# Kernel tuning notes

Measured on AMD Instinct MI355X. Metric: run time of the kernel, lower is better.

The kernel has to match this reference:

```python
import jax, jax.numpy as jnp
import numpy as np

B, T, C, H = 4, 2048, 1024, 16
D = C // H  # head_size = 64


def _layernorm(x, g, b, eps=1e-5):
    mu = jnp.mean(x, axis=-1, keepdims=True)
    var = jnp.var(x, axis=-1, keepdims=True)
    return (x - mu) * jax.lax.rsqrt(var + eps) * g + b


def setup_inputs() -> dict:
    key = jax.random.key(0)
    ks = jax.random.split(key, 12)
    s = 0.02
    return {
        "x": jax.random.normal(ks[0], (B, T, C), dtype=jnp.float32),
        "Wq": jax.random.normal(ks[1], (C, C), dtype=jnp.float32) * s,
        "Wk": jax.random.normal(ks[2], (C, C), dtype=jnp.float32) * s,
        "Wv": jax.random.normal(ks[3], (C, C), dtype=jnp.float32) * s,
        "Wo": jax.random.normal(ks[4], (C, C), dtype=jnp.float32) * s,
        "bo": jnp.zeros((C,), dtype=jnp.float32),
        "ln1_g": jnp.ones((C,), dtype=jnp.float32),
        "ln1_b": jnp.zeros((C,), dtype=jnp.float32),
        "ln2_g": jnp.ones((C,), dtype=jnp.float32),
        "ln2_b": jnp.zeros((C,), dtype=jnp.float32),
        "W1": jax.random.normal(ks[5], (C, 4 * C), dtype=jnp.float32) * s,
        "b1": jnp.zeros((4 * C,), dtype=jnp.float32),
        "W2": jax.random.normal(ks[6], (4 * C, C), dtype=jnp.float32) * s,
        "b2": jnp.zeros((C,), dtype=jnp.float32),
    }


def reference(x, Wq, Wk, Wv, Wo, bo, ln1_g, ln1_b, ln2_g, ln2_b, W1, b1, W2, b2):
    # --- self-attention branch (pre-LN) ---
    h = _layernorm(x, ln1_g, ln1_b)
    q = (h @ Wq).reshape(B, T, H, D)
    k = (h @ Wk).reshape(B, T, H, D)
    v = (h @ Wv).reshape(B, T, H, D)
    scores = jnp.einsum("bqhd,bkhd->bhqk", q, k) * (D ** -0.5)
    causal = jnp.tril(jnp.ones((T, T), dtype=bool))
    scores = jnp.where(causal, scores, -jnp.inf)
    attn = jax.nn.softmax(scores, axis=-1)  # dropout=0 in eval
    out = jnp.einsum("bhqk,bkhd->bqhd", attn, v).reshape(B, T, C)
    x = x + (out @ Wo + bo)
    # --- feed-forward branch (pre-LN) ---
    h2 = _layernorm(x, ln2_g, ln2_b)
    ff = jax.nn.relu(h2 @ W1 + b1) @ W2 + b2
    return x + ff
```

## Files before the change

### kernel.cpp

```cpp
#include <hip/hip_runtime.h>
#include <hip/hip_bf16.h>
#include <math.h>

#define Bsz 4
#define Tsz 2048
#define Csz 1024
#define Hsz 16
#define Dsz 64
#define Msz (Bsz * Tsz)

typedef __attribute__((ext_vector_type(8))) __bf16 bf16x8;
typedef __attribute__((ext_vector_type(2))) __bf16 bf16x2;
typedef __attribute__((ext_vector_type(4))) float f32x4;

#define GLOBAL_AS __attribute__((address_space(1)))
#define LDS_AS    __attribute__((address_space(3)))

#if __has_builtin(__builtin_amdgcn_exp2f)
#define EXP2F(x) __builtin_amdgcn_exp2f(x)
#define HAVE_NATIVE_EXP2 1
#else
#define HAVE_NATIVE_EXP2 0
#endif


__device__ __forceinline__ float block_sum256(float v, float* sh) {
#pragma unroll
    for (int o = 32; o > 0; o >>= 1) v += __shfl_down(v, o, 64);
    int lane = threadIdx.x & 63, w = threadIdx.x >> 6;
    __syncthreads();
    if (lane == 0) sh[w] = v;
    __syncthreads();
    return sh[0] + sh[1] + sh[2] + sh[3];
}


__global__ __launch_bounds__(256) void layernorm_bf16(const float* __restrict__ x,
                                                      const float* __restrict__ g,
                                                      const float* __restrict__ b,
                                                      __bf16* __restrict__ out) {
    __shared__ float sh[4];
    const int row = blockIdx.x;
    const float* xr = x + (size_t)row * Csz;
    float v[4];
    float s = 0.f, ss = 0.f;
#pragma unroll
    for (int i = 0; i < 4; i++) {
        v[i] = xr[threadIdx.x + i * 256];
        s += v[i];
        ss += v[i] * v[i];
    }
    float tot = block_sum256(s, sh);
    float mean = tot * (1.0f / Csz);
    float tot2 = block_sum256(ss, sh);
    float var = tot2 * (1.0f / Csz) - mean * mean;
    float inv = rsqrtf(var + 1e-5f);
    __bf16* orow = out + (size_t)row * Csz;
#pragma unroll
    for (int i = 0; i < 4; i++) {
        int c = threadIdx.x + i * 256;
        orow[c] = (__bf16)((v[i] - mean) * inv * g[c] + b[c]);
    }
}


__global__ __launch_bounds__(256) void transpose_bf16(const float* __restrict__ W,
                                                      __bf16* __restrict__ Wt,
                                                      int K, int N) {
    __shared__ float t[32][33];
    const int k0 = blockIdx.y * 32, n0 = blockIdx.x * 32;
    const int c = threadIdx.x & 31, r8 = threadIdx.x >> 5;
#pragma unroll
    for (int it = 0; it < 4; it++) {
        int r = r8 + it * 8;
        t[r][c] = W[(size_t)(k0 + r) * N + n0 + c];
    }
    __syncthreads();
#pragma unroll
    for (int it = 0; it < 4; it++) {
        int r = r8 + it * 8;
        Wt[(size_t)(n0 + r) * K + k0 + c] = (__bf16)t[c][r];
    }
}

__global__ __launch_bounds__(256) void transpose4_bf16(const float* __restrict__ Wa,
                                                       const float* __restrict__ Wb,
                                                       const float* __restrict__ Wc,
                                                       const float* __restrict__ Wd,
                                                       __bf16* __restrict__ Ta,
                                                       __bf16* __restrict__ Tb,
                                                       __bf16* __restrict__ Tc,
                                                       __bf16* __restrict__ Td) {
    __shared__ float t[32][33];
    const float* W = (blockIdx.z == 0) ? Wa : (blockIdx.z == 1) ? Wb : (blockIdx.z == 2) ? Wc : Wd;
    __bf16* Wt = (blockIdx.z == 0) ? Ta : (blockIdx.z == 1) ? Tb : (blockIdx.z == 2) ? Tc : Td;
    const int k0 = blockIdx.y * 32, n0 = blockIdx.x * 32;
    const int c = threadIdx.x & 31, r8 = threadIdx.x >> 5;
#pragma unroll
    for (int it = 0; it < 4; it++) {
        int r = r8 + it * 8;
        t[r][c] = W[(size_t)(k0 + r) * Csz + n0 + c];
    }
    __syncthreads();
#pragma unroll
    for (int it = 0; it < 4; it++) {
        int r = r8 + it * 8;
        Wt[(size_t)(n0 + r) * Csz + k0 + c] = (__bf16)t[c][r];
    }
}


__global__ __launch_bounds__(256) void gemm_bf16(const __bf16* __restrict__ A,
                                                 const __bf16* __restrict__ Bt,
                                                 float* __restrict__ Cf,
                                                 float* __restrict__ Cf2,
                                                 __bf16* __restrict__ Cb,
                                                 int M, int N, int K, int ld,
                                                 const float* __restrict__ bias,
                                                 const float* __restrict__ resid,
                                                 int do_relu) {
    __shared__ __bf16 As[128 * 64];
    __shared__ __bf16 Bs[128 * 64];

    const int tid = threadIdx.x;
    const int lane = tid & 63;
    const int w = tid >> 6;

    const int nwg = (int)(gridDim.x * gridDim.y);
    const int did = (int)(blockIdx.y * gridDim.x + blockIdx.x);
    const int work = ((nwg & 7) == 0) ? ((did & 7) * (nwg >> 3) + (did >> 3)) : did;
    const int bx = work % (int)gridDim.x;
    const int by = work / (int)gridDim.x;

    const int rowBase = by * 128;
    const int colBase = bx * 128;
    const int wr = (w & 1) * 64;
    const int wc = (w >> 1) * 64;

    const __bf16* Ak = A + (size_t)blockIdx.z * K;
    const __bf16* Bk = Bt + (size_t)blockIdx.z * K;
    float* Cfu = Cf;
    const float* residu = resid;
    const float* biasu = bias;
    if (blockIdx.z == 1) { Cfu = Cf2; residu = nullptr; biasu = nullptr; }

    const int m16 = lane & 15;
    const int kg = lane >> 4;
    const int swz = m16 & 7;

    const int sr = lane >> 3;
    const int sc = lane & 7;
    const int gcs = sc ^ sr;

    f32x4 acc[4][4] = {};

    for (int k0 = 0; k0 < K; k0 += 64) {
        __syncthreads();
#pragma unroll
        for (int it = 0; it < 4; it++) {
            int lr = w * 32 + it * 8;
            const __bf16* ga = Ak + (size_t)(rowBase + lr + sr) * ld + k0 + gcs * 8;
            __builtin_amdgcn_global_load_lds((const GLOBAL_AS unsigned int*)ga,
                                             (LDS_AS unsigned int*)(As + lr * 64),
                                             16, 0, 0);
            const __bf16* gb = Bk + (size_t)(colBase + lr + sr) * ld + k0 + gcs * 8;
            __builtin_amdgcn_global_load_lds((const GLOBAL_AS unsigned int*)gb,
                                             (LDS_AS unsigned int*)(Bs + lr * 64),
                                             16, 0, 0);
        }
        __syncthreads();

#pragma unroll
        for (int s = 0; s < 2; s++) {
            const int slot = ((s * 4 + kg) ^ swz) * 8;
            bf16x8 af[4], bfv[4];
#pragma unroll
            for (int i = 0; i < 4; i++)
                af[i] = *(const bf16x8*)(As + (wr + i * 16 + m16) * 64 + slot);
#pragma unroll
            for (int j = 0; j < 4; j++)
                bfv[j] = *(const bf16x8*)(Bs + (wc + j * 16 + m16) * 64 + slot);
#pragma unroll
            for (int i = 0; i < 4; i++)
#pragma unroll
                for (int j = 0; j < 4; j++)
                    acc[i][j] = __builtin_amdgcn_mfma_f32_16x16x32_bf16(af[i], bfv[j], acc[i][j], 0, 0, 0);
        }
    }

    const int cn = lane & 15;
    const int rq = (lane >> 4) * 4;
    float bj[4];
#pragma unroll
    for (int j = 0; j < 4; j++)
        bj[j] = biasu ? biasu[colBase + wc + j * 16 + cn] : 0.f;

#pragma unroll
    for (int i = 0; i < 4; i++) {
#pragma unroll
        for (int r = 0; r < 4; r++) {
            int m = rowBase + wr + i * 16 + rq + r;
            size_t rowOff = (size_t)m * N;
#pragma unroll
            for (int j = 0; j < 4; j++) {
                int n = colBase + wc + j * 16 + cn;
                float v = acc[i][j][r] + bj[j];
                if (do_relu) v = fmaxf(v, 0.f);
                if (residu) v += residu[rowOff + n];
                if (Cfu) Cfu[rowOff + n] = v;
                if (Cb && blockIdx.z == 0) Cb[rowOff + n] = (__bf16)v;
            }
        }
    }
}


__global__ __launch_bounds__(256) void add_partial(float* __restrict__ out,
                                                   const float* __restrict__ p,
                                                   const float* __restrict__ b2) {
    size_t i = ((size_t)blockIdx.x * 256 + threadIdx.x) * 4;
    float4 o = *(float4*)(out + i);
    const float4 a = *(const float4*)(p + i);
    const float4 bb = *(const float4*)(b2 + (i & (Csz - 1)));
    o.x += a.x + bb.x;
    o.y += a.y + bb.y;
    o.z += a.z + bb.z;
    o.w += a.w + bb.w;
    *(float4*)(out + i) = o;
}


__global__ __launch_bounds__(256, 3) void attn_mfma(const __bf16* __restrict__ QKV,
                                                    __bf16* __restrict__ O) {
    __shared__ __bf16 Ks[2][64 * 64];
    __shared__ __bf16 Vt[64 * 72];
    __shared__ __bf16 Ps[128 * 72];

    const int tid = threadIdx.x;
    const int lane = tid & 63;
    const int w = tid >> 6;
    const int bh = blockIdx.x;
    const int b = bh >> 4, h = bh & 15;
    const int qt = (int)gridDim.y - 1 - (int)blockIdx.y;
    const int qbase = qt * 128;
    const int ld3C = 3 * Csz;

    const __bf16* Qg = QKV + (size_t)(b * Tsz) * ld3C + h * Dsz;
    const __bf16* Kg = Qg + Csz;
    const __bf16* Vg = Qg + 2 * Csz;

    const int m16 = lane & 15;
    const int kg = lane >> 4;
    const int rq = kg * 4;
    const int wrow = w * 32;
    const int swz = m16 & 7;

    bf16x8 aq[2][2];
#pragma unroll
    for (int i = 0; i < 2; i++)
#pragma unroll
        for (int s = 0; s < 2; s++)
            aq[i][s] = *(const bf16x8*)(Qg + (size_t)(qbase + wrow + i * 16 + m16) * ld3C + (s * 4 + kg) * 8);

    const int sr = lane >> 3;
    const int sc = lane & 7;
    const int gcs = sc ^ sr;

    const int kp = (lane & 31) * 2;
    const int dg = w * 2 + (lane >> 5);

    f32x4 Oacc[2][4];
    float l_part[2][4];
#pragma unroll
    for (int i = 0; i < 2; i++)
#pragma unroll
        for (int j = 0; j < 4; j++) Oacc[i][j] = (f32x4){0.f, 0.f, 0.f, 0.f};
#pragma unroll
    for (int i = 0; i < 2; i++)
#pragma unroll
        for (int r = 0; r < 4; r++) l_part[i][r] = 0.f;

    const float CEXP = 0.18033688f;
    const int nkt = 2 * qt + 2;

#pragma unroll
    for (int it = 0; it < 2; it++) {
        int lr = w * 16 + it * 8 + sr;
        const __bf16* src = Kg + (size_t)lr * ld3C + gcs * 8;
        __builtin_amdgcn_global_load_lds((const GLOBAL_AS unsigned int*)src,
                                         (LDS_AS unsigned int*)(&Ks[0][(w * 16 + it * 8) * 64]),
                                         16, 0, 0);
    }
    bf16x8 vc0 = *(const bf16x8*)(Vg + (size_t)kp * ld3C + dg * 8);
    bf16x8 vc1 = *(const bf16x8*)(Vg + (size_t)(kp + 1) * ld3C + dg * 8);
    bf16x8 vn0, vn1;

    for (int kt = 0; kt < nkt; kt++) {
        const int cur = kt & 1;
        const int kbase = kt * 64;

        if (kt + 1 < nkt) {
            const int nb = kbase + 64;
#pragma unroll
            for (int it = 0; it < 2; it++) {
                int lr = w * 16 + it * 8 + sr;
                const __bf16* src = Kg + (size_t)(nb + lr) * ld3C + gcs * 8;
                __builtin_amdgcn_global_load_lds((const GLOBAL_AS unsigned int*)src,
                                                 (LDS_AS unsigned int*)(&Ks[cur ^ 1][(w * 16 + it * 8) * 64]),
                                                 16, 0, 0);
            }
            vn0 = *(const bf16x8*)(Vg + (size_t)(nb + kp) * ld3C + dg * 8);
            vn1 = *(const bf16x8*)(Vg + (size_t)(nb + kp + 1) * ld3C + dg * 8);
            asm volatile("s_waitcnt vmcnt(4)" ::: "memory");
        } else {
            asm volatile("s_waitcnt vmcnt(0)" ::: "memory");
        }
        __builtin_amdgcn_s_barrier();

        f32x4 S[2][4];
#pragma unroll
        for (int i = 0; i < 2; i++)
#pragma unroll
            for (int j = 0; j < 4; j++) S[i][j] = (f32x4){0.f, 0.f, 0.f, 0.f};
#pragma unroll
        for (int s = 0; s < 2; s++) {
            bf16x8 bk[4];
#pragma unroll
            for (int j = 0; j < 4; j++)
                bk[j] = *(const bf16x8*)(&Ks[cur][(j * 16 + m16) * 64 + (((s * 4 + kg) ^ swz) * 8)]);
            __builtin_amdgcn_s_setprio(1);
#pragma unroll
            for (int i = 0; i < 2; i++)
#pragma unroll
                for (int j = 0; j < 4; j++)
                    S[i][j] = __builtin_amdgcn_mfma_f32_16x16x32_bf16(aq[i][s], bk[j], S[i][j], 0, 0, 0);
            __builtin_amdgcn_s_setprio(0);
        }

        if (kt >= 2 * qt) {
#pragma unroll
            for (int i = 0; i < 2; i++)
#pragma unroll
                for (int j = 0; j < 4; j++)
#pragma unroll
                    for (int r = 0; r < 4; r++) {
                        float arg = S[i][j][r] * CEXP;
                        if (kbase + j * 16 + m16 > qbase + wrow + i * 16 + rq + r)
                            arg = -INFINITY;
#if HAVE_NATIVE_EXP2
                        float e = EXP2F(arg);
#else
                        float e = __expf(arg * 0.6931472f);
#endif
                        S[i][j][r] = e;
                        l_part[i][r] += e;
                    }
        } else {
#pragma unroll
            for (int i = 0; i < 2; i++)
#pragma unroll
                for (int j = 0; j < 4; j++)
#pragma unroll
                    for (int r = 0; r < 4; r++) {
                        float arg = S[i][j][r] * CEXP;
#if HAVE_NATIVE_EXP2
                        float e = EXP2F(arg);
#else
                        float e = __expf(arg * 0.6931472f);
#endif
                        S[i][j][r] = e;
                        l_part[i][r] += e;
                    }
        }

#pragma unroll
        for (int i = 0; i < 2; i++)
#pragma unroll
            for (int j = 0; j < 4; j++)
#pragma unroll
                for (int r = 0; r < 4; r++)
                    Ps[(wrow + i * 16 + rq + r) * 72 + j * 16 + m16] = (__bf16)S[i][j][r];
#pragma unroll
        for (int e = 0; e < 8; e++) {
            bf16x2 pr;
            pr[0] = vc0[e];
            pr[1] = vc1[e];
            *(bf16x2*)(Vt + (dg * 8 + e) * 72 + kp) = pr;
        }
        asm volatile("s_waitcnt lgkmcnt(0)" ::: "memory");
        __builtin_amdgcn_s_barrier();

#pragma unroll
        for (int s = 0; s < 2; s++) {
            bf16x8 ap[2], bv[4];
#pragma unroll
            for (int i = 0; i < 2; i++)
                ap[i] = *(const bf16x8*)(Ps + (wrow + i * 16 + m16) * 72 + s * 32 + kg * 8);
#pragma unroll
            for (int j = 0; j < 4; j++)
                bv[j] = *(const bf16x8*)(Vt + (j * 16 + m16) * 72 + s * 32 + kg * 8);
            __builtin_amdgcn_s_setprio(1);
#pragma unroll
            for (int i = 0; i < 2; i++)
#pragma unroll
                for (int j = 0; j < 4; j++)
                    Oacc[i][j] = __builtin_amdgcn_mfma_f32_16x16x32_bf16(ap[i], bv[j], Oacc[i][j], 0, 0, 0);
            __builtin_amdgcn_s_setprio(0);
        }

        if (kt + 1 < nkt) { vc0 = vn0; vc1 = vn1; }
    }

#pragma unroll
    for (int i = 0; i < 2; i++) {
#pragma unroll
        for (int r = 0; r < 4; r++) {
            float l = l_part[i][r];
#pragma unroll
            for (int msk = 1; msk < 16; msk <<= 1) l += __shfl_xor(l, msk, 64);
            const float inv = 1.0f / l;
            const int qrow = qbase + wrow + i * 16 + rq + r;
            __bf16* orow = O + (size_t)(b * Tsz + qrow) * Csz + h * Dsz;
#pragma unroll
            for (int j = 0; j < 4; j++)
                orow[j * 16 + m16] = (__bf16)(Oacc[i][j][r] * inv);
        }
    }
}


extern "C" void kernel_launch(void* const* d_in, const int* in_sizes, int n_in,
                              void* d_out, int out_size, void* d_ws, size_t ws_size,
                              hipStream_t stream) {
    const float* x     = (const float*)d_in[0];
    const float* Wq    = (const float*)d_in[1];
    const float* Wk    = (const float*)d_in[2];
    const float* Wv    = (const float*)d_in[3];
    const float* Wo    = (const float*)d_in[4];
    const float* bo    = (const float*)d_in[5];
    const float* ln1_g = (const float*)d_in[6];
    const float* ln1_b = (const float*)d_in[7];
    const float* ln2_g = (const float*)d_in[8];
    const float* ln2_b = (const float*)d_in[9];
    const float* W1    = (const float*)d_in[10];
    const float* b1    = (const float*)d_in[11];
    const float* W2    = (const float*)d_in[12];
    const float* b2    = (const float*)d_in[13];
    float* out = (float*)d_out;

    const size_t MB = 1u << 20;
    char* w = (char*)d_ws;
    __bf16* h    = (__bf16*)(w + 0);
    __bf16* Wqkv = (__bf16*)(w + 16 * MB);
    __bf16* Wot  = (__bf16*)(w + 22 * MB);
    __bf16* W1t  = (__bf16*)(w + 24 * MB);
    __bf16* W2t  = (__bf16*)(w + 32 * MB);
    __bf16* QKVb = (__bf16*)(w + 40 * MB);
    __bf16* AO   = (__bf16*)(w + 88 * MB);
    __bf16* ff1  = (__bf16*)(w + 40 * MB);
    float*  p1   = (float*)(w + 0);

    transpose4_bf16<<<dim3(32, 32, 4), 256, 0, stream>>>(Wq, Wk, Wv, Wo,
                                                         Wqkv, Wqkv + 1024 * 1024, Wqkv + 2048 * 1024, Wot);
    transpose_bf16<<<dim3(4 * Csz / 32, Csz / 32), 256, 0, stream>>>(W1, W1t, Csz, 4 * Csz);
    transpose_bf16<<<dim3(Csz / 32, 4 * Csz / 32), 256, 0, stream>>>(W2, W2t, 4 * Csz, Csz);

    layernorm_bf16<<<Msz, 256, 0, stream>>>(x, ln1_g, ln1_b, h);
    gemm_bf16<<<dim3(3 * Csz / 128, Msz / 128), 256, 0, stream>>>(
        h, Wqkv, nullptr, nullptr, QKVb, Msz, 3 * Csz, Csz, Csz, nullptr, nullptr, 0);
    attn_mfma<<<dim3(Bsz * Hsz, Tsz / 128), 256, 0, stream>>>(QKVb, AO);
    gemm_bf16<<<dim3(Csz / 128, Msz / 128), 256, 0, stream>>>(
        AO, Wot, out, nullptr, nullptr, Msz, Csz, Csz, Csz, bo, x, 0);

    layernorm_bf16<<<Msz, 256, 0, stream>>>(out, ln2_g, ln2_b, h);
    gemm_bf16<<<dim3(4 * Csz / 128, Msz / 128), 256, 0, stream>>>(
        h, W1t, nullptr, nullptr, ff1, Msz, 4 * Csz, Csz, Csz, b1, nullptr, 1);
    gemm_bf16<<<dim3(Csz / 128, Msz / 128, 2), 256, 0, stream>>>(
        ff1, W2t, out, p1, nullptr, Msz, Csz, 2 * Csz, 4 * Csz, nullptr, out, 0);
    add_partial<<<Msz * Csz / 1024, 256, 0, stream>>>(out, p1, b2);
}
```

Measured before the change: 540.3 us.

## Add 256x256-tile 8-wave GEMM with interleaved staging for QKV and FFN GEMMs

Introduces a new GEMM kernel with 256x256 output tiles, 512 threads, double-buffered LDS filled by direct global-to-LDS loads, and an 8-phase schedule that interleaves staging of the next K-tile with MFMA work. It also remaps workgroups in an XCD-aware order. It replaces the 128x128 GEMM for the QKV projection, FFN up-projection and split-K FFN down-projection, aiming for more data reuse per loaded tile and better overlap of loads with compute. The larger tiles give fewer workgroups, which risks poorer occupancy, tail effects and higher register pressure. The output projection GEMM keeps the old kernel.

```diff
diff --git a/kernel.cpp b/kernel.cpp
--- a/kernel.cpp
+++ b/kernel.cpp
@@ -215,6 +215,144 @@
 }
 
 
+#define Tile256 (256 * 64)
+
+#define STAGE_A6(kt, hh) do {                                                      \
+    const int bbuf_ = (kt) & 1;                                                    \
+    _Pragma("unroll") for (int l_ = 0; l_ < 2; l_++) {                             \
+        const int lr_ = (hh) * 128 + w * 16 + l_ * 8;                              \
+        const __bf16* ga_ = Ak + (size_t)(rowBase + lr_ + sr) * ld + (kt) * 64 + gcs * 8; \
+        __builtin_amdgcn_global_load_lds((const GLOBAL_AS unsigned int*)ga_,       \
+            (LDS_AS unsigned int*)(As + bbuf_ * Tile256 + lr_ * 64), 16, 0, 0);    \
+    } } while (0)
+
+#define STAGE_B6(kt, hh) do {                                                      \
+    const int bbuf_ = (kt) & 1;                                                    \
+    _Pragma("unroll") for (int l_ = 0; l_ < 2; l_++) {                             \
+        const int lr_ = (hh) * 128 + w * 16 + l_ * 8;                              \
+        const __bf16* gb_ = Bk + (size_t)(colBase + lr_ + sr) * ld + (kt) * 64 + gcs * 8; \
+        __builtin_amdgcn_global_load_lds((const GLOBAL_AS unsigned int*)gb_,       \
+            (LDS_AS unsigned int*)(Bs + bbuf_ * Tile256 + lr_ * 64), 16, 0, 0);    \
+    } } while (0)
+
+#define PHASE6(ks, q, bufc, STAGES, VMW) do {                                      \
+    bf16x8 af[4];                                                                  \
+    _Pragma("unroll") for (int i_ = 0; i_ < 4; i_++)                               \
+        af[i_] = *(const bf16x8*)(As + (bufc) * Tile256 +                          \
+                  (wm * 128 + ((q) * 4 + i_) * 16 + m16) * 64 +                    \
+                  ((((ks) * 4 + kg) ^ swz) * 8));                                  \
+    if ((q) == 0) {                                                                \
+        _Pragma("unroll") for (int j_ = 0; j_ < 4; j_++)                           \
+            bv[j_] = *(const bf16x8*)(Bs + (bufc) * Tile256 +                      \
+                      (wn * 64 + j_ * 16 + m16) * 64 +                             \
+                      ((((ks) * 4 + kg) ^ swz) * 8));                              \
+    }                                                                              \
+    STAGES;                                                                        \
+    VMW;                                                                           \
+    __builtin_amdgcn_s_barrier();                                                  \
+    __builtin_amdgcn_s_setprio(1);                                                 \
+    _Pragma("unroll") for (int i_ = 0; i_ < 4; i_++)                               \
+        _Pragma("unroll") for (int j_ = 0; j_ < 4; j_++)                           \
+            acc[(q) * 4 + i_][j_] = __builtin_amdgcn_mfma_f32_16x16x32_bf16(       \
+                af[i_], bv[j_], acc[(q) * 4 + i_][j_], 0, 0, 0);                   \
+    __builtin_amdgcn_s_setprio(0);                                                 \
+    __builtin_amdgcn_s_barrier();                                                  \
+} while (0)
+
+__global__ __launch_bounds__(512, 2) void gemm256(const __bf16* __restrict__ A,
+                                                  const __bf16* __restrict__ Bt,
+                                                  float* __restrict__ Cf,
+                                                  float* __restrict__ Cf2,
+                                                  __bf16* __restrict__ Cb,
+                                                  int M, int N, int K, int ld,
+                                                  const float* __restrict__ bias,
+                                                  const float* __restrict__ resid,
+                                                  int do_relu) {
+    __shared__ __bf16 As[2 * Tile256];
+    __shared__ __bf16 Bs[2 * Tile256];
+
+    const int tid = threadIdx.x;
+    const int lane = tid & 63;
+    const int w = tid >> 6;
+    const int wm = w >> 2;
+    const int wn = w & 3;
+
+    const int nwg = (int)(gridDim.x * gridDim.y);
+    const int did = (int)(blockIdx.y * gridDim.x + blockIdx.x);
+    const int work = ((nwg & 7) == 0) ? ((did & 7) * (nwg >> 3) + (did >> 3)) : did;
+    const int bx = work % (int)gridDim.x;
+    const int by = work / (int)gridDim.x;
+    const int rowBase = by * 256;
+    const int colBase = bx * 256;
+
+    const __bf16* Ak = A + (size_t)blockIdx.z * K;
+    const __bf16* Bk = Bt + (size_t)blockIdx.z * K;
+    float* Cfu = Cf;
+    const float* residu = resid;
+    const float* biasu = bias;
+    if (blockIdx.z == 1) { Cfu = Cf2; residu = nullptr; biasu = nullptr; }
+
+    const int m16 = lane & 15;
+    const int kg = lane >> 4;
+    const int swz = m16 & 7;
+    const int sr = lane >> 3;
+    const int sc = lane & 7;
+    const int gcs = sc ^ sr;
+
+    const int nt = K >> 6;
+
+    f32x4 acc[8][4] = {};
+    bf16x8 bv[4];
+
+    STAGE_A6(0, 0); STAGE_B6(0, 0); STAGE_A6(0, 1); STAGE_B6(0, 1);
+    STAGE_B6(1, 0);
+    asm volatile("s_waitcnt vmcnt(2)" ::: "memory");
+    __builtin_amdgcn_s_barrier();
+
+    for (int t0 = 0; t0 < nt; t0 += 2) {
+        const bool p2 = (t0 + 2 < nt);
+        const bool p3 = (t0 + 3 < nt);
+        PHASE6(0, 0, 0, STAGE_A6(t0 + 1, 0), );
+        PHASE6(0, 1, 0, STAGE_B6(t0 + 1, 1), );
+        PHASE6(1, 0, 0, STAGE_A6(t0 + 1, 1), );
+        PHASE6(1, 1, 0, if (p2) STAGE_B6(t0 + 2, 0),
+               if (p2) asm volatile("s_waitcnt vmcnt(2)" ::: "memory");
+               else    asm volatile("s_waitcnt vmcnt(0)" ::: "memory"));
+        PHASE6(0, 0, 1, if (p2) STAGE_A6(t0 + 2, 0), );
+        PHASE6(0, 1, 1, if (p2) STAGE_B6(t0 + 2, 1), );
+        PHASE6(1, 0, 1, if (p2) STAGE_A6(t0 + 2, 1), );
+        PHASE6(1, 1, 1, if (p3) STAGE_B6(t0 + 3, 0),
+               if (p3) asm volatile("s_waitcnt vmcnt(2)" ::: "memory");
+               else    asm volatile("s_waitcnt vmcnt(0)" ::: "memory"));
+    }
+
+    const int cn = lane & 15;
+    const int rqe = (lane >> 4) * 4;
+    float bj[4];
+#pragma unroll
+    for (int j = 0; j < 4; j++)
+        bj[j] = biasu ? biasu[colBase + wn * 64 + j * 16 + cn] : 0.f;
+
+#pragma unroll
+    for (int mi = 0; mi < 8; mi++) {
+#pragma unroll
+        for (int r = 0; r < 4; r++) {
+            const int m = rowBase + wm * 128 + mi * 16 + rqe + r;
+            const size_t rowOff = (size_t)m * N;
+#pragma unroll
+            for (int j = 0; j < 4; j++) {
+                const int n = colBase + wn * 64 + j * 16 + cn;
+                float v = acc[mi][j][r] + bj[j];
+                if (do_relu) v = fmaxf(v, 0.f);
+                if (residu) v += residu[rowOff + n];
+                if (Cfu) Cfu[rowOff + n] = v;
+                if (Cb && blockIdx.z == 0) Cb[rowOff + n] = (__bf16)v;
+            }
+        }
+    }
+}
+
+
 __global__ __launch_bounds__(256) void add_partial(float* __restrict__ out,
                                                    const float* __restrict__ p,
                                                    const float* __restrict__ b2) {
@@ -392,19 +530,19 @@
 
 #pragma unroll
         for (int s = 0; s < 2; s++) {
-            bf16x8 ap[2], bv[4];
+            bf16x8 ap[2], bvv[4];
 #pragma unroll
             for (int i = 0; i < 2; i++)
                 ap[i] = *(const bf16x8*)(Ps + (wrow + i * 16 + m16) * 72 + s * 32 + kg * 8);
 #pragma unroll
             for (int j = 0; j < 4; j++)
-                bv[j] = *(const bf16x8*)(Vt + (j * 16 + m16) * 72 + s * 32 + kg * 8);
+                bvv[j] = *(const bf16x8*)(Vt + (j * 16 + m16) * 72 + s * 32 + kg * 8);
             __builtin_amdgcn_s_setprio(1);
 #pragma unroll
             for (int i = 0; i < 2; i++)
 #pragma unroll
                 for (int j = 0; j < 4; j++)
-                    Oacc[i][j] = __builtin_amdgcn_mfma_f32_16x16x32_bf16(ap[i], bv[j], Oacc[i][j], 0, 0, 0);
+                    Oacc[i][j] = __builtin_amdgcn_mfma_f32_16x16x32_bf16(ap[i], bvv[j], Oacc[i][j], 0, 0, 0);
             __builtin_amdgcn_s_setprio(0);
         }
 
@@ -466,16 +604,16 @@
     transpose_bf16<<<dim3(Csz / 32, 4 * Csz / 32), 256, 0, stream>>>(W2, W2t, 4 * Csz, Csz);
 
     layernorm_bf16<<<Msz, 256, 0, stream>>>(x, ln1_g, ln1_b, h);
-    gemm_bf16<<<dim3(3 * Csz / 128, Msz / 128), 256, 0, stream>>>(
+    gemm256<<<dim3(3 * Csz / 256, Msz / 256), 512, 0, stream>>>(
         h, Wqkv, nullptr, nullptr, QKVb, Msz, 3 * Csz, Csz, Csz, nullptr, nullptr, 0);
     attn_mfma<<<dim3(Bsz * Hsz, Tsz / 128), 256, 0, stream>>>(QKVb, AO);
     gemm_bf16<<<dim3(Csz / 128, Msz / 128), 256, 0, stream>>>(
         AO, Wot, out, nullptr, nullptr, Msz, Csz, Csz, Csz, bo, x, 0);
 
     layernorm_bf16<<<Msz, 256, 0, stream>>>(out, ln2_g, ln2_b, h);
-    gemm_bf16<<<dim3(4 * Csz / 128, Msz / 128), 256, 0, stream>>>(
+    gemm256<<<dim3(4 * Csz / 256, Msz / 256), 512, 0, stream>>>(
         h, W1t, nullptr, nullptr, ff1, Msz, 4 * Csz, Csz, Csz, b1, nullptr, 1);
-    gemm_bf16<<<dim3(Csz / 128, Msz / 128, 2), 256, 0, stream>>>(
+    gemm256<<<dim3(Csz / 256, Msz / 256, 2), 512, 0, stream>>>(
         ff1, W2t, out, p1, nullptr, Msz, Csz, 2 * Csz, 4 * Csz, nullptr, out, 0);
     add_partial<<<Msz * Csz / 1024, 256, 0, stream>>>(out, p1, b2);
 }
```

Result: faster. 524.4 us, median of 2 (-3.0%).
